# Performance work log

Hardware: AMD Instinct MI355X
Metric: run time of the kernel (lower is better)

## Reference

```python
import jax, jax.numpy as jnp
import numpy as np

N_NODES = 50000
N_EDGES = 800000
IN_CH = 128
H1, C1 = 8, 16      # conv1: 8 heads x 16 channels, concat -> 128
H2, C2 = 1, 64      # conv2: 1 head x 64 channels, mean (concat=False)
NEG_SLOPE = 0.2


def setup_inputs() -> dict:
    key = jax.random.key(0)
    ks = jax.random.split(key, 10)
    x = jax.random.normal(ks[0], (N_NODES, IN_CH), dtype=jnp.float32)
    edge_index = jax.random.randint(ks[1], (2, N_EDGES), 0, N_NODES, dtype=jnp.int64)
    s1 = 1.0 / np.sqrt(IN_CH)
    s2 = 1.0 / np.sqrt(H1 * C1)
    W1 = jax.random.normal(ks[2], (IN_CH, H1 * C1), dtype=jnp.float32) * s1
    att_src1 = jax.random.normal(ks[3], (H1, C1), dtype=jnp.float32) * s1
    att_dst1 = jax.random.normal(ks[4], (H1, C1), dtype=jnp.float32) * s1
    b1 = jnp.zeros((H1 * C1,), dtype=jnp.float32)
    W2 = jax.random.normal(ks[5], (H1 * C1, H2 * C2), dtype=jnp.float32) * s2
    att_src2 = jax.random.normal(ks[6], (H2, C2), dtype=jnp.float32) * s2
    att_dst2 = jax.random.normal(ks[7], (H2, C2), dtype=jnp.float32) * s2
    b2 = jnp.zeros((C2,), dtype=jnp.float32)
    return {"x": x, "edge_index": edge_index, "W1": W1, "att_src1": att_src1,
            "att_dst1": att_dst1, "b1": b1, "W2": W2, "att_src2": att_src2,
            "att_dst2": att_dst2, "b2": b2}


def gat_conv(x, src, dst, W, att_src, att_dst, bias, heads, out_ch, concat):
    # x: [N, F_in]; src/dst: [E'] (self-loops already appended)
    N = x.shape[0]
    h = (x @ W).reshape(N, heads, out_ch)                     # [N, H, C]
    a_s = jnp.sum(h * att_src[None], axis=-1)                 # [N, H]
    a_d = jnp.sum(h * att_dst[None], axis=-1)                 # [N, H]
    logits = jax.nn.leaky_relu(a_s[src] + a_d[dst], NEG_SLOPE)  # [E', H]
    # segment softmax over edges grouped by destination node
    m = jax.ops.segment_max(logits, dst, num_segments=N)       # [N, H]
    e = jnp.exp(logits - m[dst])                               # [E', H]
    denom = jax.ops.segment_sum(e, dst, num_segments=N)        # [N, H]
    alpha = e / (denom[dst] + 1e-16)                           # [E', H]
    msg = h[src] * alpha[:, :, None]                           # [E', H, C]
    out = jax.ops.segment_sum(msg, dst, num_segments=N)        # [N, H, C]
    if concat:
        out = out.reshape(N, heads * out_ch)
    else:
        out = out.mean(axis=1)
    return out + bias


def reference(x, edge_index, W1, att_src1, att_dst1, b1, W2, att_src2, att_dst2, b2):
    N = x.shape[0]
    loop = jnp.arange(N, dtype=edge_index.dtype)
    src = jnp.concatenate([edge_index[0], loop])   # GATConv adds self-loops
    dst = jnp.concatenate([edge_index[1], loop])
    # eval mode: all dropouts are identity
    h = gat_conv(x, src, dst, W1, att_src1, att_dst1, b1, H1, C1, concat=True)
    h = jax.nn.elu(h)
    out = gat_conv(h, src, dst, W2, att_src2, att_dst2, b2, H2, C2, concat=False)
    return jax.nn.log_softmax(out, axis=1)
```

## Files before the change

kernel.cpp:

```cpp
#include <hip/hip_runtime.h>
#include <math.h>

#define IN_CH 128
#define H1N 8
#define C1N 16
#define C2N 64
#define NEG_SLOPE 0.2f

#define BKT_SHIFT 7
#define BKT_NODES (1 << BKT_SHIFT)
#define NBLK 128

typedef unsigned short ushortT;

__device__ __forceinline__ ushortT f2bf(float f) {
    unsigned u = __float_as_uint(f);
    unsigned r = u + 0x7FFFu + ((u >> 16) & 1u);
    return (ushortT)(r >> 16);
}
__device__ __forceinline__ float bf2f(ushortT b) {
    return __uint_as_float(((unsigned)b) << 16);
}
__device__ __forceinline__ float leaky(float x) {
    return (x > 0.f) ? x : NEG_SLOPE * x;
}


__global__ __launch_bounds__(512) void k_cnt(const int* __restrict__ src,
                                             const int* __restrict__ dst,
                                             int E, int N, int* __restrict__ cnt) {
    __shared__ int hist[512];
    int blk = blockIdx.x, t = threadIdx.x;
    int nb = (N + BKT_NODES - 1) >> BKT_SHIFT;
    if (t < nb) hist[t] = 0;
    __syncthreads();
    int Etot = E + N;
    int chunk = (Etot + gridDim.x - 1) / gridDim.x;
    int lo = blk * chunk;
    int hi = lo + chunk; if (hi > Etot) hi = Etot;
    for (int i = lo + t; i < hi; i += 512) {
        int d = (i < E) ? dst[i] : (i - E);
        atomicAdd(&hist[d >> BKT_SHIFT], 1);
    }
    __syncthreads();
    if (t < nb) cnt[t * NBLK + blk] = hist[t];
}

__global__ __launch_bounds__(NBLK) void k_scanrel(int* __restrict__ cnt,
                                                  int* __restrict__ bucketTotal) {
    __shared__ int sh[NBLK];
    int b = blockIdx.x, t = threadIdx.x;
    sh[t] = cnt[b * NBLK + t];
    __syncthreads();
    for (int off = 1; off < NBLK; off <<= 1) {
        int v = (t >= off) ? sh[t - off] : 0;
        __syncthreads();
        sh[t] += v;
        __syncthreads();
    }
    if (t == NBLK - 1) bucketTotal[b] = sh[t];
    cnt[b * NBLK + t] = (t == 0) ? 0 : sh[t - 1];
}

__global__ __launch_bounds__(512) void k_scanbucket(const int* __restrict__ bucketTotal,
                                                    int nb, int* __restrict__ bBase,
                                                    int N, int* __restrict__ offsets) {
    __shared__ int sh[512];
    int t = threadIdx.x;
    sh[t] = (t < nb) ? bucketTotal[t] : 0;
    __syncthreads();
    for (int off = 1; off < 512; off <<= 1) {
        int v = (t >= off) ? sh[t - off] : 0;
        __syncthreads();
        sh[t] += v;
        __syncthreads();
    }
    if (t < nb) bBase[t] = (t == 0) ? 0 : sh[t - 1];
    if (t == 511) { bBase[nb] = sh[511]; offsets[N] = sh[511]; }
}

__global__ __launch_bounds__(512) void k_bin(const int* __restrict__ src,
                                             const int* __restrict__ dst,
                                             int E, int N,
                                             const int* __restrict__ cnt,
                                             const int* __restrict__ bBase,
                                             unsigned* __restrict__ pair) {
    __shared__ int cur[512];
    int blk = blockIdx.x, t = threadIdx.x;
    int nb = (N + BKT_NODES - 1) >> BKT_SHIFT;
    if (t < nb) cur[t] = bBase[t] + cnt[t * NBLK + blk];
    __syncthreads();
    int Etot = E + N;
    int chunk = (Etot + gridDim.x - 1) / gridDim.x;
    int lo = blk * chunk;
    int hi = lo + chunk; if (hi > Etot) hi = Etot;
    for (int i = lo + t; i < hi; i += 512) {
        int s, d;
        if (i < E) { s = src[i]; d = dst[i]; }
        else       { s = d = i - E; }
        int b = d >> BKT_SHIFT;
        int pos = atomicAdd(&cur[b], 1);
        pair[pos] = ((unsigned)(d & (BKT_NODES - 1)) << 16) | (unsigned)s;
    }
}

__global__ __launch_bounds__(256) void k_csr_local(const unsigned* __restrict__ pair,
                                                   const int* __restrict__ bBase,
                                                   int N, int* __restrict__ offsets,
                                                   ushortT* __restrict__ csr) {
    __shared__ int hist[BKT_NODES];
    __shared__ int loff[BKT_NODES];
    int b = blockIdx.x;
    int t = threadIdx.x;
    int base = bBase[b];
    int cnt = bBase[b + 1] - base;
    const unsigned* pp = pair + base;

    if (t < BKT_NODES) hist[t] = 0;
    __syncthreads();
    for (int i = t; i < cnt; i += 256) atomicAdd(&hist[pp[i] >> 16], 1);
    __syncthreads();
    if (t < BKT_NODES) loff[t] = hist[t];
    __syncthreads();
    for (int off = 1; off < BKT_NODES; off <<= 1) {
        int v = 0;
        if (t < BKT_NODES && t >= off) v = loff[t - off];
        __syncthreads();
        if (t < BKT_NODES) loff[t] += v;
        __syncthreads();
    }
    int node0 = b << BKT_SHIFT;
    if (t < BKT_NODES) {
        int excl = (t == 0) ? 0 : loff[t - 1];
        hist[t] = excl;
        int g = node0 + t;
        if (g < N) offsets[g] = base + excl;
    }
    __syncthreads();
    for (int i = t; i < cnt; i += 256) {
        unsigned pk = pp[i];
        int pos = atomicAdd(&hist[pk >> 16], 1);
        csr[base + pos] = (ushortT)(pk & 0xFFFFu);
    }
}


template <int KOUT, int HEADS, bool BFIN>
__global__ __launch_bounds__(256) void k_gemm_att(const void* __restrict__ Av,
                                                  const float* __restrict__ W,
                                                  const float* __restrict__ att_s,
                                                  const float* __restrict__ att_d,
                                                  int N, ushortT* __restrict__ Cbf,
                                                  float* __restrict__ as_,
                                                  float* __restrict__ ad_) {
    constexpr int CG  = KOUT / 4;
    constexpr int TY  = 256 / CG;
    constexpr int RPT = 64 / TY;
    constexpr int RW  = (KOUT / HEADS) / 4;
    static_assert(RW == 4 || RW == 16, "reduce width");
    __shared__ float As[64][16];
    __shared__ float Ws[16][KOUT];
    int t = threadIdx.x;
    int row0 = blockIdx.x * 64;
    int tx = t % CG, ty = t / CG;

    float4 acc[RPT];
#pragma unroll
    for (int i = 0; i < RPT; ++i) acc[i] = make_float4(0.f, 0.f, 0.f, 0.f);

    for (int k0 = 0; k0 < IN_CH; k0 += 16) {
        {
            int r  = t >> 2;
            int cc = (t & 3) * 4;
            int gr = row0 + r;
            float4 v = make_float4(0.f, 0.f, 0.f, 0.f);
            if (gr < N) {
                if constexpr (BFIN) {
                    const ushortT* A = (const ushortT*)Av;
                    ushort4 u = *(const ushort4*)(A + (size_t)gr * IN_CH + k0 + cc);
                    v.x = bf2f(u.x); v.y = bf2f(u.y); v.z = bf2f(u.z); v.w = bf2f(u.w);
                } else {
                    const float* A = (const float*)Av;
                    v = *(const float4*)(A + (size_t)gr * IN_CH + k0 + cc);
                }
            }
            *(float4*)(&As[r][cc]) = v;
        }
        {
            constexpr int TOT = 16 * KOUT / 4;
            for (int idx = t; idx < TOT; idx += 256) {
                int rr = idx / (KOUT / 4);
                int cc = (idx % (KOUT / 4)) * 4;
                *(float4*)(&Ws[rr][cc]) = *(const float4*)(W + (size_t)(k0 + rr) * KOUT + cc);
            }
        }
        __syncthreads();
#pragma unroll
        for (int kk = 0; kk < 16; ++kk) {
            float4 w = *(const float4*)(&Ws[kk][tx * 4]);
#pragma unroll
            for (int i = 0; i < RPT; ++i) {
                float a = As[ty * RPT + i][kk];
                acc[i].x += a * w.x; acc[i].y += a * w.y;
                acc[i].z += a * w.z; acc[i].w += a * w.w;
            }
        }
        __syncthreads();
    }

    float4 s4 = *(const float4*)(att_s + tx * 4);
    float4 d4 = *(const float4*)(att_d + tx * 4);
#pragma unroll
    for (int i = 0; i < RPT; ++i) {
        int gr = row0 + ty * RPT + i;
        float as = acc[i].x * s4.x + acc[i].y * s4.y + acc[i].z * s4.z + acc[i].w * s4.w;
        float ad = acc[i].x * d4.x + acc[i].y * d4.y + acc[i].z * d4.z + acc[i].w * d4.w;
#pragma unroll
        for (int o = 1; o < RW; o <<= 1) {
            as += __shfl_xor(as, o);
            ad += __shfl_xor(ad, o);
        }
        if (gr < N) {
            ushort4 pk;
            pk.x = f2bf(acc[i].x); pk.y = f2bf(acc[i].y);
            pk.z = f2bf(acc[i].z); pk.w = f2bf(acc[i].w);
            *(ushort4*)(Cbf + (size_t)gr * KOUT + tx * 4) = pk;
            if ((tx % RW) == 0) {
                int h = tx / RW;
                as_[(size_t)gr * HEADS + h] = as;
                ad_[(size_t)gr * HEADS + h] = ad;
            }
        }
    }
}


__global__ void k_agg1(const ushortT* __restrict__ h1bf,
                       const float* __restrict__ as1, const float* __restrict__ ad1,
                       const int* __restrict__ offsets, const ushortT* __restrict__ csr,
                       const float* __restrict__ b1,
                       int N, ushortT* __restrict__ h2in) {
    int wid  = (blockIdx.x * blockDim.x + threadIdx.x) >> 6;
    int lane = threadIdx.x & 63;
    if (wid >= N) return;
    int v = wid;
    int hc = lane >> 3;
    int hp = lane & 7;
    float adc = ad1[v * H1N + hc];
    float adp = ad1[v * H1N + hp];
    float denom = 0.f, acc0 = 0.f, acc1 = 0.f;
    int beg = offsets[v], end = offsets[v + 1];
    int j = beg;
    for (; j + 8 <= end; j += 8) {
        int ep = lane >> 3;
        int sE = csr[j + ep];
        float a = as1[sE * H1N + hp];
        float pp = __expf(leaky(a + adp));
#pragma unroll
        for (int e = 0; e < 8; ++e) {
            int srcl = e * 8 + hc;
            float pe = __shfl(pp, srcl);
            int   se = __shfl(sE, srcl);
            unsigned q = *(const unsigned*)(h1bf + (size_t)se * IN_CH + lane * 2);
            denom += pe;
            acc0 = fmaf(pe, bf2f((ushortT)(q & 0xFFFFu)), acc0);
            acc1 = fmaf(pe, bf2f((ushortT)(q >> 16)), acc1);
        }
    }
    if (j + 4 <= end) {
        int ep = (lane >> 3) & 3;
        int sE = csr[j + ep];
        float a = as1[sE * H1N + hp];
        float pp = __expf(leaky(a + adp));
#pragma unroll
        for (int e = 0; e < 4; ++e) {
            int srcl = e * 8 + hc;
            float pe = __shfl(pp, srcl);
            int   se = __shfl(sE, srcl);
            unsigned q = *(const unsigned*)(h1bf + (size_t)se * IN_CH + lane * 2);
            denom += pe;
            acc0 = fmaf(pe, bf2f((ushortT)(q & 0xFFFFu)), acc0);
            acc1 = fmaf(pe, bf2f((ushortT)(q >> 16)), acc1);
        }
        j += 4;
    }
    for (; j < end; ++j) {
        int s = csr[j];
        float a = as1[s * H1N + hc];
        unsigned q = *(const unsigned*)(h1bf + (size_t)s * IN_CH + lane * 2);
        float p = __expf(leaky(a + adc));
        denom += p;
        acc0 = fmaf(p, bf2f((ushortT)(q & 0xFFFFu)), acc0);
        acc1 = fmaf(p, bf2f((ushortT)(q >> 16)), acc1);
    }
    float inv = 1.f / (denom + 1e-16f);
    float o0 = acc0 * inv + b1[lane * 2];
    float o1 = acc1 * inv + b1[lane * 2 + 1];
    o0 = (o0 > 0.f) ? o0 : expm1f(o0);
    o1 = (o1 > 0.f) ? o1 : expm1f(o1);
    unsigned pk = ((unsigned)f2bf(o1) << 16) | (unsigned)f2bf(o0);
    *(unsigned*)(h2in + (size_t)v * IN_CH + lane * 2) = pk;
}


__global__ __launch_bounds__(256) void k_agg2(const ushortT* __restrict__ h2bf,
                       const float* __restrict__ as2, const float* __restrict__ ad2,
                       const int* __restrict__ offsets, const ushortT* __restrict__ csr,
                       const float* __restrict__ b2,
                       int N, float* __restrict__ out) {
    int wid  = (blockIdx.x * blockDim.x + threadIdx.x) >> 6;
    int lane = threadIdx.x & 63;
    int half = lane >> 5;
    int v = wid * 2 + half;
    bool alive = (v < N);
    int c2 = (lane & 31) * 2;

    float ad = 0.f;
    int beg = 0, end = 0;
    if (alive) {
        ad = ad2[v];
        beg = offsets[v];
        end = offsets[v + 1];
    }
    float denom = 0.f, acc0 = 0.f, acc1 = 0.f;
    int j = beg;
    for (; j + 8 <= end; j += 8) {
        int sE = csr[j + (lane & 7)];
        float p = __expf(leaky(as2[sE] + ad));
#pragma unroll
        for (int e = 0; e < 8; ++e) {
            int srcl = (lane & 32) + e;
            float pe = __shfl(p, srcl);
            int   se = __shfl(sE, srcl);
            unsigned q = *(const unsigned*)(h2bf + (size_t)se * C2N + c2);
            denom += pe;
            acc0 = fmaf(pe, bf2f((ushortT)(q & 0xFFFFu)), acc0);
            acc1 = fmaf(pe, bf2f((ushortT)(q >> 16)), acc1);
        }
    }
    if (j < end) {
        int m = end - j;
        int ep = lane & 7;
        int sE = 0;
        float p = 0.f;
        if (ep < m) {
            sE = csr[j + ep];
            p = __expf(leaky(as2[sE] + ad));
        }
        for (int e = 0; e < m; ++e) {
            int srcl = (lane & 32) + e;
            float pe = __shfl(p, srcl);
            int   se = __shfl(sE, srcl);
            unsigned q = *(const unsigned*)(h2bf + (size_t)se * C2N + c2);
            denom += pe;
            acc0 = fmaf(pe, bf2f((ushortT)(q & 0xFFFFu)), acc0);
            acc1 = fmaf(pe, bf2f((ushortT)(q >> 16)), acc1);
        }
    }
    float inv = 1.f / (denom + 1e-16f);
    float o0 = acc0 * inv + b2[c2];
    float o1 = acc1 * inv + b2[c2 + 1];
    float mx = fmaxf(o0, o1);
#pragma unroll
    for (int off = 16; off >= 1; off >>= 1) mx = fmaxf(mx, __shfl_xor(mx, off));
    float se2 = __expf(o0 - mx) + __expf(o1 - mx);
#pragma unroll
    for (int off = 16; off >= 1; off >>= 1) se2 += __shfl_xor(se2, off);
    if (alive) {
        float lse = logf(se2);
        float2 ov; ov.x = o0 - mx - lse; ov.y = o1 - mx - lse;
        *(float2*)(out + (size_t)v * C2N + c2) = ov;
    }
}


extern "C" void kernel_launch(void* const* d_in, const int* in_sizes, int n_in,
                              void* d_out, int out_size, void* d_ws, size_t ws_size,
                              hipStream_t stream) {
    const float* x      = (const float*)d_in[0];
    const int*   ei     = (const int*)d_in[1];
    const float* W1     = (const float*)d_in[2];
    const float* att_s1 = (const float*)d_in[3];
    const float* att_d1 = (const float*)d_in[4];
    const float* b1     = (const float*)d_in[5];
    const float* W2     = (const float*)d_in[6];
    const float* att_s2 = (const float*)d_in[7];
    const float* att_d2 = (const float*)d_in[8];
    const float* b2     = (const float*)d_in[9];

    int N = in_sizes[0] / IN_CH;
    int E = in_sizes[1] / 2;
    const int* srcA = ei;
    const int* dstA = ei + E;
    int Etot = E + N;
    int nb = (N + BKT_NODES - 1) >> BKT_SHIFT;

    char* p = (char*)d_ws;
    auto carve = [&](size_t bytes) {
        void* r = (void*)p;
        p += (bytes + 255) & ~(size_t)255;
        return r;
    };
    ushortT* h1bf = (ushortT*)carve((size_t)N * IN_CH * 2);
    ushortT* h2bf = (ushortT*)carve((size_t)N * C2N * 2);
    ushortT* h2in = (ushortT*)carve((size_t)N * IN_CH * 2);
    float* as1  = (float*)carve((size_t)N * H1N * 4);
    float* ad1  = (float*)carve((size_t)N * H1N * 4);
    float* as2  = (float*)carve((size_t)N * 4);
    float* ad2  = (float*)carve((size_t)N * 4);
    int* offsets     = (int*)carve((size_t)(N + 1) * 4);
    ushortT* csr     = (ushortT*)carve((size_t)(Etot + 16) * 2);
    int* cnt         = (int*)carve((size_t)nb * NBLK * 4);
    int* bucketTotal = (int*)carve((size_t)nb * 4);
    int* bBase       = (int*)carve((size_t)(nb + 1) * 4);
    unsigned* pair   = (unsigned*)carve((size_t)Etot * 4);

    k_cnt<<<NBLK, 512, 0, stream>>>(srcA, dstA, E, N, cnt);
    k_scanrel<<<nb, NBLK, 0, stream>>>(cnt, bucketTotal);
    k_scanbucket<<<1, 512, 0, stream>>>(bucketTotal, nb, bBase, N, offsets);
    k_bin<<<NBLK, 512, 0, stream>>>(srcA, dstA, E, N, cnt, bBase, pair);
    k_csr_local<<<nb, 256, 0, stream>>>(pair, bBase, N, offsets, csr);

    k_gemm_att<128, 8, false><<<(N + 63) / 64, 256, 0, stream>>>(x, W1, att_s1, att_d1,
                                                                 N, h1bf, as1, ad1);
    k_agg1<<<(N * 64 + 255) / 256, 256, 0, stream>>>(h1bf, as1, ad1, offsets, csr, b1, N, h2in);

    k_gemm_att<64, 1, true><<<(N + 63) / 64, 256, 0, stream>>>(h2in, W2, att_s2, att_d2,
                                                               N, h2bf, as2, ad2);
    k_agg2<<<(N * 32 + 255) / 256, 256, 0, stream>>>(h2bf, as2, ad2, offsets, csr, b2,
                                                     N, (float*)d_out);
}
```

Baseline: 148.7 us.

## Rewrite projection GEMM with bf16 MFMA and fused attention-score epilogue

Replaces the fp32 SIMT tiled GEMM in both GAT layers with a bf16 MFMA 16x16x32 kernel. The full 64-row A tile and the transposed W are staged in LDS once. The attention source and destination dot products are computed from the MFMA accumulators using cross-lane shuffles. The goal is to cut the FMA-bound GEMM cost. The trade-offs are bf16 rounding of the fp32 input x and W in layer 1, and an uncoalesced transposed W load and scalar bf16 output stores done per block.

```diff
diff --git a/kernel.cpp b/kernel.cpp
--- a/kernel.cpp
+++ b/kernel.cpp
@@ -12,6 +12,8 @@
 #define NBLK 128
 
 typedef unsigned short ushortT;
+typedef short bf16x8 __attribute__((ext_vector_type(8)));
+typedef float f32x4 __attribute__((ext_vector_type(4)));
 
 __device__ __forceinline__ ushortT f2bf(float f) {
     unsigned u = __float_as_uint(f);
@@ -153,83 +155,106 @@
                                                   int N, ushortT* __restrict__ Cbf,
                                                   float* __restrict__ as_,
                                                   float* __restrict__ ad_) {
-    constexpr int CG  = KOUT / 4;
-    constexpr int TY  = 256 / CG;
-    constexpr int RPT = 64 / TY;
-    constexpr int RW  = (KOUT / HEADS) / 4;
-    static_assert(RW == 4 || RW == 16, "reduce width");
-    __shared__ float As[64][16];
-    __shared__ float Ws[16][KOUT];
+    constexpr int NT = KOUT / 16;
+    constexpr int LDK = IN_CH + 8;
+    __shared__ ushortT Alds[64][LDK];
+    __shared__ ushortT Wlds[KOUT][LDK];
     int t = threadIdx.x;
     int row0 = blockIdx.x * 64;
-    int tx = t % CG, ty = t / CG;
-
-    float4 acc[RPT];
-#pragma unroll
-    for (int i = 0; i < RPT; ++i) acc[i] = make_float4(0.f, 0.f, 0.f, 0.f);
-
-    for (int k0 = 0; k0 < IN_CH; k0 += 16) {
-        {
-            int r  = t >> 2;
-            int cc = (t & 3) * 4;
-            int gr = row0 + r;
-            float4 v = make_float4(0.f, 0.f, 0.f, 0.f);
-            if (gr < N) {
-                if constexpr (BFIN) {
-                    const ushortT* A = (const ushortT*)Av;
-                    ushort4 u = *(const ushort4*)(A + (size_t)gr * IN_CH + k0 + cc);
-                    v.x = bf2f(u.x); v.y = bf2f(u.y); v.z = bf2f(u.z); v.w = bf2f(u.w);
-                } else {
-                    const float* A = (const float*)Av;
-                    v = *(const float4*)(A + (size_t)gr * IN_CH + k0 + cc);
-                }
+    int w    = t >> 6;
+    int lane = t & 63;
+    int lm   = lane & 15;
+    int lg   = lane >> 4;
+
+    for (int idx = t; idx < 64 * 32; idx += 256) {
+        int r  = idx >> 5;
+        int c4 = (idx & 31) << 2;
+        int gr = row0 + r;
+        ushort4 u; u.x = 0; u.y = 0; u.z = 0; u.w = 0;
+        if (gr < N) {
+            if constexpr (BFIN) {
+                u = *(const ushort4*)((const ushortT*)Av + (size_t)gr * IN_CH + c4);
+            } else {
+                float4 v = *(const float4*)((const float*)Av + (size_t)gr * IN_CH + c4);
+                u.x = f2bf(v.x); u.y = f2bf(v.y); u.z = f2bf(v.z); u.w = f2bf(v.w);
             }
-            *(float4*)(&As[r][cc]) = v;
-        }
-        {
-            constexpr int TOT = 16 * KOUT / 4;
-            for (int idx = t; idx < TOT; idx += 256) {
-                int rr = idx / (KOUT / 4);
-                int cc = (idx % (KOUT / 4)) * 4;
-                *(float4*)(&Ws[rr][cc]) = *(const float4*)(W + (size_t)(k0 + rr) * KOUT + cc);
+        }
+        *(ushort4*)(&Alds[r][c4]) = u;
+    }
+    for (int idx = t; idx < IN_CH * KOUT; idx += 256) {
+        int k = idx / KOUT;
+        int n = idx % KOUT;
+        Wlds[n][k] = f2bf(W[(size_t)k * KOUT + n]);
+    }
+    __syncthreads();
+
+    f32x4 acc[NT];
+#pragma unroll
+    for (int ct = 0; ct < NT; ++ct) acc[ct] = (f32x4){0.f, 0.f, 0.f, 0.f};
+
+    int ar = w * 16 + lm;
+#pragma unroll
+    for (int ks = 0; ks < 4; ++ks) {
+        int kb = ks * 32 + lg * 8;
+        bf16x8 af = *(const bf16x8*)(&Alds[ar][kb]);
+#pragma unroll
+        for (int ct = 0; ct < NT; ++ct) {
+            bf16x8 bf = *(const bf16x8*)(&Wlds[ct * 16 + lm][kb]);
+            acc[ct] = __builtin_amdgcn_mfma_f32_16x16x32_bf16(af, bf, acc[ct], 0, 0, 0);
+        }
+    }
+
+    float asp0 = 0.f, asp1 = 0.f, asp2 = 0.f, asp3 = 0.f;
+    float adp0 = 0.f, adp1 = 0.f, adp2 = 0.f, adp3 = 0.f;
+#pragma unroll
+    for (int ct = 0; ct < NT; ++ct) {
+        int gcol = ct * 16 + lm;
+        float sc = att_s[gcol];
+        float dc = att_d[gcol];
+        float c0 = acc[ct][0], c1 = acc[ct][1], c2 = acc[ct][2], c3 = acc[ct][3];
+#pragma unroll
+        for (int i = 0; i < 4; ++i) {
+            int gr = row0 + w * 16 + lg * 4 + i;
+            if (gr < N) Cbf[(size_t)gr * KOUT + gcol] = f2bf(acc[ct][i]);
+        }
+        if constexpr (HEADS == 1) {
+            asp0 = fmaf(c0, sc, asp0); asp1 = fmaf(c1, sc, asp1);
+            asp2 = fmaf(c2, sc, asp2); asp3 = fmaf(c3, sc, asp3);
+            adp0 = fmaf(c0, dc, adp0); adp1 = fmaf(c1, dc, adp1);
+            adp2 = fmaf(c2, dc, adp2); adp3 = fmaf(c3, dc, adp3);
+        } else {
+            float r0 = c0 * sc, r1 = c1 * sc, r2 = c2 * sc, r3 = c3 * sc;
+            float q0 = c0 * dc, q1 = c1 * dc, q2 = c2 * dc, q3 = c3 * dc;
+#pragma unroll
+            for (int off = 1; off < 16; off <<= 1) {
+                r0 += __shfl_xor(r0, off); r1 += __shfl_xor(r1, off);
+                r2 += __shfl_xor(r2, off); r3 += __shfl_xor(r3, off);
+                q0 += __shfl_xor(q0, off); q1 += __shfl_xor(q1, off);
+                q2 += __shfl_xor(q2, off); q3 += __shfl_xor(q3, off);
             }
-        }
-        __syncthreads();
-#pragma unroll
-        for (int kk = 0; kk < 16; ++kk) {
-            float4 w = *(const float4*)(&Ws[kk][tx * 4]);
-#pragma unroll
-            for (int i = 0; i < RPT; ++i) {
-                float a = As[ty * RPT + i][kk];
-                acc[i].x += a * w.x; acc[i].y += a * w.y;
-                acc[i].z += a * w.z; acc[i].w += a * w.w;
+            if (lm == 0) {
+                int grb = row0 + w * 16 + lg * 4;
+                if (grb + 0 < N) { as_[(size_t)(grb + 0) * HEADS + ct] = r0; ad_[(size_t)(grb + 0) * HEADS + ct] = q0; }
+                if (grb + 1 < N) { as_[(size_t)(grb + 1) * HEADS + ct] = r1; ad_[(size_t)(grb + 1) * HEADS + ct] = q1; }
+                if (grb + 2 < N) { as_[(size_t)(grb + 2) * HEADS + ct] = r2; ad_[(size_t)(grb + 2) * HEADS + ct] = q2; }
+                if (grb + 3 < N) { as_[(size_t)(grb + 3) * HEADS + ct] = r3; ad_[(size_t)(grb + 3) * HEADS + ct] = q3; }
             }
         }
-        __syncthreads();
-    }
-
-    float4 s4 = *(const float4*)(att_s + tx * 4);
-    float4 d4 = *(const float4*)(att_d + tx * 4);
-#pragma unroll
-    for (int i = 0; i < RPT; ++i) {
-        int gr = row0 + ty * RPT + i;
-        float as = acc[i].x * s4.x + acc[i].y * s4.y + acc[i].z * s4.z + acc[i].w * s4.w;
-        float ad = acc[i].x * d4.x + acc[i].y * d4.y + acc[i].z * d4.z + acc[i].w * d4.w;
-#pragma unroll
-        for (int o = 1; o < RW; o <<= 1) {
-            as += __shfl_xor(as, o);
-            ad += __shfl_xor(ad, o);
-        }
-        if (gr < N) {
-            ushort4 pk;
-            pk.x = f2bf(acc[i].x); pk.y = f2bf(acc[i].y);
-            pk.z = f2bf(acc[i].z); pk.w = f2bf(acc[i].w);
-            *(ushort4*)(Cbf + (size_t)gr * KOUT + tx * 4) = pk;
-            if ((tx % RW) == 0) {
-                int h = tx / RW;
-                as_[(size_t)gr * HEADS + h] = as;
-                ad_[(size_t)gr * HEADS + h] = ad;
-            }
+    }
+    if constexpr (HEADS == 1) {
+#pragma unroll
+        for (int off = 1; off < 16; off <<= 1) {
+            asp0 += __shfl_xor(asp0, off); asp1 += __shfl_xor(asp1, off);
+            asp2 += __shfl_xor(asp2, off); asp3 += __shfl_xor(asp3, off);
+            adp0 += __shfl_xor(adp0, off); adp1 += __shfl_xor(adp1, off);
+            adp2 += __shfl_xor(adp2, off); adp3 += __shfl_xor(adp3, off);
+        }
+        if (lm == 0) {
+            int grb = row0 + w * 16 + lg * 4;
+            if (grb + 0 < N) { as_[grb + 0] = asp0; ad_[grb + 0] = adp0; }
+            if (grb + 1 < N) { as_[grb + 1] = asp1; ad_[grb + 1] = adp1; }
+            if (grb + 2 < N) { as_[grb + 2] = asp2; ad_[grb + 2] = adp2; }
+            if (grb + 3 < N) { as_[grb + 3] = asp3; ad_[grb + 3] = adp3; }
         }
     }
 }
@@ -409,7 +434,7 @@
     float* as2  = (float*)carve((size_t)N * 4);
     float* ad2  = (float*)carve((size_t)N * 4);
     int* offsets     = (int*)carve((size_t)(N + 1) * 4);
-    ushortT* csr     = (ushortT*)carve((size_t)(Etot + 16) * 2);
+    ushortT* csr     = (ushortT*)carve((size_t)(Etot + 32) * 2);
     int* cnt         = (int*)carve((size_t)nb * NBLK * 4);
     int* bucketTotal = (int*)carve((size_t)nb * 4);
     int* bBase       = (int*)carve((size_t)(nb + 1) * 4);
```

New measurement: 138.2 us. 7.1% less time.
